# Performance work log

Hardware: AMD Instinct MI355X
Metric: run time of the kernel (lower is better)

The kernel has to match this reference:

```python
import jax, jax.numpy as jnp
import numpy as np


def setup_inputs() -> dict:
    key = jax.random.key(0)
    ks = jax.random.split(key, 7)
    B, D, d1, d2, d3 = 256, 256, 1024, 512, 256
    s = lambda f: 1.0 / np.sqrt(f)  # torch nn.Linear-style init scale
    return {
        "x": jax.random.normal(ks[0], (B, D), jnp.float32),
        "W1": jax.random.normal(ks[1], (d1, D), jnp.float32) * s(D),
        "b1": jax.random.normal(ks[2], (d1,), jnp.float32) * s(D),
        "W2": jax.random.normal(ks[3], (d2, d1), jnp.float32) * s(d1),
        "b2": jax.random.normal(ks[4], (d2,), jnp.float32) * s(d1),
        "W3": jax.random.normal(ks[5], (d3, d2), jnp.float32) * s(d2),
        "b3": jax.random.normal(ks[6], (d3,), jnp.float32) * s(d2),
        "k": 10,
    }


def _border_dists(x, W1, b1, W2, b2, W3, b3):
    # Layer 1: pre-activations and boundary distances. For the first layer the
    # effective linear map is W1 itself (shared across the batch).
    z1 = x @ W1.T + b1                                   # [B, d1]
    dist1 = jnp.abs(z1) / jnp.linalg.norm(W1, axis=1)    # [B, d1]
    m1 = (z1 > 0).astype(x.dtype)
    V1 = m1[:, :, None] * W1[None]                       # [B, d1, D] per-instance map after ReLU
    h1 = m1 * z1

    # Layer 2
    z2 = h1 @ W2.T + b2                                  # [B, d2]
    V2 = jnp.einsum('oi,bid->bod', W2, V1)               # [B, d2, D]
    dist2 = jnp.abs(z2) / jnp.linalg.norm(V2, axis=2)
    m2 = (z2 > 0).astype(x.dtype)
    h2 = m2 * z2

    # Layer 3
    z3 = h2 @ W3.T + b3                                  # [B, d3]
    V3 = jnp.einsum('oi,bid->bod', W3, m2[:, :, None] * V2)  # [B, d3, D]
    dist3 = jnp.abs(z3) / jnp.linalg.norm(V3, axis=2)

    return jnp.concatenate([dist1, dist2, dist3], axis=1)  # [B, d1+d2+d3]


def reference(x, W1, b1, W2, b2, W3, b3, k):
    dists = _border_dists(x, W1, b1, W2, b2, W3, b3)
    # smallest-k distances per instance via top_k on negated distances
    neg_top, _ = jax.lax.top_k(-dists, k)                # [B, k]
    return jnp.sum(-neg_top)                             # border-distance loss (scalar)
```

## Files before the change

kernel.cpp:

```cpp
#include <hip/hip_runtime.h>
#include <math.h>
#include <float.h>

#define B   256
#define D   256
#define D1  1024
#define D2  512
#define D3  256
#define NDIST (D1 + D2 + D3)
#define CQ  2.0f

typedef __attribute__((ext_vector_type(8))) short short8;
typedef __attribute__((ext_vector_type(4))) float f32x4;
typedef __attribute__((ext_vector_type(4))) int   i32x4;

__device__ __forceinline__ float waveReduceSum(float v) {
    #pragma unroll
    for (int off = 32; off > 0; off >>= 1)
        v += __shfl_down(v, off, 64);
    return v;
}
__device__ __forceinline__ float waveReduceMax(float v) {
    #pragma unroll
    for (int off = 32; off > 0; off >>= 1)
        v = fmaxf(v, __shfl_down(v, off, 64));
    return v;
}
__device__ __forceinline__ unsigned short f2bf(float f) {
    unsigned int u = __float_as_uint(f);
    u = (u + 0x7FFFu + ((u >> 16) & 1u)) >> 16;
    return (unsigned short)u;
}
__device__ __forceinline__ float bf2f(unsigned short h) {
    return __uint_as_float(((unsigned int)h) << 16);
}
__device__ __forceinline__ void gld16(const void* g, void* l) {
    __builtin_amdgcn_global_load_lds(
        (const __attribute__((address_space(1))) unsigned int*)g,
        (__attribute__((address_space(3))) unsigned int*)l, 16, 0, 0);
}
__device__ __forceinline__ int swz_src(int row, int lane) {
    return ((lane & 3) + ((row >> 1) & 3)) & 3;
}
__device__ __forceinline__ int swz_frag(int row, int quad) {
    return row * 32 + (((quad - ((row >> 1) & 3)) & 3) * 8);
}

__device__ __forceinline__ void split_job(const float* src, unsigned short* hi,
                                          unsigned short* lo, int off) {
    float4 v = *(const float4*)(src + off);
    ushort4 h, l;
    h.x = f2bf(v.x); l.x = f2bf(v.x - bf2f(h.x));
    h.y = f2bf(v.y); l.y = f2bf(v.y - bf2f(h.y));
    h.z = f2bf(v.z); l.z = f2bf(v.z - bf2f(h.z));
    h.w = f2bf(v.w); l.w = f2bf(v.w - bf2f(h.w));
    *(ushort4*)(hi + off) = h;
    *(ushort4*)(lo + off) = l;
}

__global__ __launch_bounds__(256) void k_prepA(
    const float* __restrict__ x, const float* __restrict__ W1,
    unsigned short* __restrict__ xhi,  unsigned short* __restrict__ xlo,
    unsigned short* __restrict__ W1hi, unsigned short* __restrict__ W1lo,
    float* __restrict__ rn1) {
    int blk = blockIdx.x;
    int t = threadIdx.x;
    if (blk < 64) {
        split_job(x, xhi, xlo, blk * 1024 + t * 4);
        return;
    }
    if (blk < 320) {
        split_job(W1, W1hi, W1lo, (blk - 64) * 1024 + t * 4);
        return;
    }
    {
        int gw = (blk - 320) * 4 + (t >> 6);
        int lane = t & 63;
        const float* row = W1 + (size_t)gw * D;
        float s = 0.f;
        for (int tt = lane; tt < D; tt += 64) { float v = row[tt]; s += v * v; }
        s = waveReduceSum(s);
        if (lane == 0) rn1[gw] = sqrtf(s);
    }
}

template <int KD, int KL>
__device__ __forceinline__ void mfma3_64(
    const unsigned short* __restrict__ Ahi, const unsigned short* __restrict__ Alo,
    const unsigned short* __restrict__ Bhi, const unsigned short* __restrict__ Blo,
    int m0, int n0, int k0, unsigned short* sm, f32x4 acc[2][2]) {
    int tid = threadIdx.x;
    int l = tid & 63, w = tid >> 6;
    int rsub = l >> 2;
    int quad = l >> 4, l16 = l & 15;
    int wm = (w >> 1) * 32, wn = (w & 1) * 32;
    unsigned short* sAh = sm;
    unsigned short* sAl = sm + 2048;
    unsigned short* sBh = sm + 4096;
    unsigned short* sBl = sm + 6144;
    ptrdiff_t dA = Alo - Ahi, dB = Blo - Bhi;
    int rloc = w * 16 + rsub;
    int c = swz_src(rloc, l);
    const unsigned short* pa = Ahi + (size_t)(m0 + rloc) * KD + k0 + c * 8;
    const unsigned short* pb = Bhi + (size_t)(n0 + rloc) * KD + k0 + c * 8;
    int aoff[2], boff[2];
    #pragma unroll
    for (int mt = 0; mt < 2; mt++) aoff[mt] = swz_frag(wm + mt * 16 + l16, quad);
    #pragma unroll
    for (int nt = 0; nt < 2; nt++) boff[nt] = swz_frag(wn + nt * 16 + l16, quad);
    for (int kk = 0; kk < KL; kk += 32) {
        gld16(pa + kk,      sAh + w * 512);
        gld16(pa + dA + kk, sAl + w * 512);
        gld16(pb + kk,      sBh + w * 512);
        gld16(pb + dB + kk, sBl + w * 512);
        __syncthreads();
        short8 ah[2], al[2], bh[2], bl[2];
        #pragma unroll
        for (int mt = 0; mt < 2; mt++) {
            ah[mt] = *(const short8*)(sAh + aoff[mt]);
            al[mt] = *(const short8*)(sAl + aoff[mt]);
        }
        #pragma unroll
        for (int nt = 0; nt < 2; nt++) {
            bh[nt] = *(const short8*)(sBh + boff[nt]);
            bl[nt] = *(const short8*)(sBl + boff[nt]);
        }
        #pragma unroll
        for (int mt = 0; mt < 2; mt++)
            #pragma unroll
            for (int nt = 0; nt < 2; nt++) {
                acc[mt][nt] = __builtin_amdgcn_mfma_f32_16x16x32_bf16(ah[mt], bh[nt], acc[mt][nt], 0, 0, 0);
                acc[mt][nt] = __builtin_amdgcn_mfma_f32_16x16x32_bf16(ah[mt], bl[nt], acc[mt][nt], 0, 0, 0);
                acc[mt][nt] = __builtin_amdgcn_mfma_f32_16x16x32_bf16(al[mt], bh[nt], acc[mt][nt], 0, 0, 0);
            }
        __syncthreads();
    }
}

__global__ __launch_bounds__(256) void k_l1p(
    const float* __restrict__ W1, const float* __restrict__ W2,
    const float* __restrict__ W3,
    const unsigned short* __restrict__ xhi,  const unsigned short* __restrict__ xlo,
    const unsigned short* __restrict__ W1hi, const unsigned short* __restrict__ W1lo,
    const float* __restrict__ b1, const float* __restrict__ rn1,
    float* __restrict__ dists, unsigned char* __restrict__ m1q,
    unsigned short* __restrict__ h1hi, unsigned short* __restrict__ h1lo,
    float* __restrict__ zeros, float* __restrict__ outp,
    unsigned short* __restrict__ W2hi, unsigned short* __restrict__ W2lo,
    unsigned short* __restrict__ W3hi, unsigned short* __restrict__ W3lo,
    signed char* __restrict__ W1Ti8, float* __restrict__ saq,
    signed char* __restrict__ W2i8,  float* __restrict__ sbq,
    signed char* __restrict__ W3i8,  float* __restrict__ s3q) {
    __shared__ __align__(16) unsigned short sm[8192];
    int blk = blockIdx.x;
    int t = threadIdx.x;

    if (blk < 64) {
        int m0 = (blk & 3) * 64, n0 = (blk >> 2) * 64;
        f32x4 acc[2][2] = {};
        mfma3_64<D, D>(xhi, xlo, W1hi, W1lo, m0, n0, 0, sm, acc);
        int l = t & 63, w = t >> 6;
        int quad = l >> 4, l16 = l & 15;
        int wm = (w >> 1) * 32, wn = (w & 1) * 32;
        #pragma unroll
        for (int mt = 0; mt < 2; mt++)
            #pragma unroll
            for (int nt = 0; nt < 2; nt++) {
                int n = n0 + wn + nt * 16 + l16;
                float bv = b1[n], rv = rn1[n];
                #pragma unroll
                for (int r = 0; r < 4; r++) {
                    int m = m0 + wm + mt * 16 + quad * 4 + r;
                    float z = acc[mt][nt][r] + bv;
                    size_t idx = (size_t)m * D1 + n;
                    dists[idx] = fabsf(z) / rv;
                    m1q[idx] = (z > 0.f) ? 0xFFu : 0u;
                    float h = z > 0.f ? z : 0.f;
                    unsigned short hh = f2bf(h);
                    h1hi[idx] = hh;
                    h1lo[idx] = f2bf(h - bf2f(hh));
                }
            }
        return;
    }
    if (blk < 448) {
        if (blk == 64 && t == 0) outp[0] = 0.f;
        int i4 = (blk - 64) * 1024 + t * 4;
        *(float4*)(zeros + i4) = make_float4(0.f, 0.f, 0.f, 0.f);
        return;
    }
    if (blk < 960) {
        split_job(W2, W2hi, W2lo, (blk - 448) * 1024 + t * 4);
        return;
    }
    if (blk < 1088) {
        split_job(W3, W3hi, W3lo, (blk - 960) * 1024 + t * 4);
        return;
    }
    if (blk < 1120) {
        int ty = t >> 5, tx = t & 31;
        int d = (blk - 1088) * 8 + ty;
        float m = 0.f;
        for (int i = tx; i < D1; i += 32) m = fmaxf(m, fabsf(W1[(size_t)i * D + d]));
        #pragma unroll
        for (int off = 16; off > 0; off >>= 1) m = fmaxf(m, __shfl_down(m, off, 32));
        m = __shfl(m, 0, 32);
        m = fmaxf(m, 1e-20f);
        if (tx == 0) saq[d] = m / 127.f;
        float inv = 127.f / m;
        for (int i = tx; i < D1; i += 32) {
            int q = __float2int_rn(W1[(size_t)i * D + d] * inv);
            W1Ti8[(size_t)d * D1 + i] = (signed char)q;
        }
        return;
    }
    if (blk < 1248) {
        int o = (blk - 1120) * 4 + (t >> 6);
        int l = t & 63;
        const float* row = W2 + (size_t)o * D1;
        float m = 0.f;
        for (int tt = l; tt < D1; tt += 64) m = fmaxf(m, fabsf(row[tt]));
        m = waveReduceMax(m);
        m = __shfl(m, 0, 64);
        m = fmaxf(m, 1e-20f);
        if (l == 0) sbq[o] = m / 127.f;
        float inv = 127.f / m;
        for (int tt = l; tt < D1; tt += 64)
            W2i8[(size_t)o * D1 + tt] = (signed char)__float2int_rn(row[tt] * inv);
        return;
    }
    {
        int p = (blk - 1248) * 4 + (t >> 6);
        int l = t & 63;
        const float* row = W3 + (size_t)p * D2;
        float m = 0.f;
        for (int tt = l; tt < D2; tt += 64) m = fmaxf(m, fabsf(row[tt]));
        m = waveReduceMax(m);
        m = __shfl(m, 0, 64);
        m = fmaxf(m, 1e-20f);
        if (l == 0) s3q[p] = m / 127.f;
        float inv = 127.f / m;
        for (int tt = l; tt < D2; tt += 64)
            W3i8[(size_t)p * D2 + tt] = (signed char)__float2int_rn(row[tt] * inv);
    }
}

__global__ __launch_bounds__(256) void k_big1(
    const unsigned short* __restrict__ h1hi, const unsigned short* __restrict__ h1lo,
    const unsigned short* __restrict__ W2hi, const unsigned short* __restrict__ W2lo,
    float* __restrict__ z2,
    const signed char* __restrict__ W1Ti8,
    const signed char* __restrict__ W2i8,
    const unsigned char* __restrict__ m1q,
    const float* __restrict__ saq,
    const float* __restrict__ sbq,
    signed char* __restrict__ qV2,
    float* __restrict__ norm2) {
    __shared__ __align__(16) unsigned char smem[32768];
    int bid = blockIdx.x;

    if (bid < 128) {
        unsigned short* sm = (unsigned short*)smem;
        int m0 = (bid & 3) * 64, n0 = ((bid >> 2) & 7) * 64, k0 = (bid >> 5) * 256;
        f32x4 acc[2][2] = {};
        mfma3_64<D1, 256>(h1hi, h1lo, W2hi, W2lo, m0, n0, k0, sm, acc);
        int l = threadIdx.x & 63, w = threadIdx.x >> 6;
        int quad = l >> 4, l16 = l & 15;
        int wm = (w >> 1) * 32, wn = (w & 1) * 32;
        #pragma unroll
        for (int mt = 0; mt < 2; mt++)
            #pragma unroll
            for (int nt = 0; nt < 2; nt++) {
                int n = n0 + wn + nt * 16 + l16;
                #pragma unroll
                for (int r = 0; r < 4; r++) {
                    int m = m0 + wm + mt * 16 + quad * 4 + r;
                    atomicAdd(&z2[(size_t)m * D2 + n], acc[mt][nt][r]);
                }
            }
        return;
    }

    int j = bid - 128;
    signed char* As = (signed char*)smem;
    signed char* Bs = (signed char*)smem + 16384;
    int m0 = (j & 1) * 128;
    int o0 = ((j >> 1) & 3) * 128;
    int b = j >> 3;
    int tid = threadIdx.x;
    int l = tid & 63, w = tid >> 6;
    int quad = l >> 4, l16 = l & 15;
    int wm = (w >> 1) * 64, wn = (w & 1) * 64;
    const unsigned char* mrow = m1q + (size_t)b * D1;

    const signed char* pa[4];
    const signed char* pb[4];
    int lrow = l >> 3, ls = l & 7;
    #pragma unroll
    for (int r = 0; r < 4; r++) {
        int row = r * 32 + w * 8 + lrow;
        int c = (ls + (row & 7)) & 7;
        pa[r] = W1Ti8 + (size_t)(m0 + row) * D1 + c * 16;
        pb[r] = W2i8 + (size_t)(o0 + row) * D1 + c * 16;
    }
    int aoff[4][2], boff[4][2];
    #pragma unroll
    for (int mt = 0; mt < 4; mt++) {
        int tr = wm + mt * 16 + l16;
        #pragma unroll
        for (int ks = 0; ks < 2; ks++)
            aoff[mt][ks] = tr * 128 + (((ks * 4 + quad) - (tr & 7)) & 7) * 16;
    }
    #pragma unroll
    for (int nt = 0; nt < 4; nt++) {
        int tr = wn + nt * 16 + l16;
        #pragma unroll
        for (int ks = 0; ks < 2; ks++)
            boff[nt][ks] = tr * 128 + (((ks * 4 + quad) - (tr & 7)) & 7) * 16;
    }

    i32x4 acc[4][4];
    #pragma unroll
    for (int i = 0; i < 4; i++)
        #pragma unroll
        for (int jj = 0; jj < 4; jj++) acc[i][jj] = (i32x4)0;

    for (int kk = 0; kk < D1; kk += 128) {
        #pragma unroll
        for (int r = 0; r < 4; r++) {
            gld16(pa[r] + kk, As + r * 4096 + w * 1024);
            gld16(pb[r] + kk, Bs + r * 4096 + w * 1024);
        }
        i32x4 mv0 = *(const i32x4*)(mrow + kk + quad * 16);
        i32x4 mv1 = *(const i32x4*)(mrow + kk + 64 + quad * 16);
        __syncthreads();
        #pragma unroll
        for (int ks = 0; ks < 2; ks++) {
            i32x4 mv = ks ? mv1 : mv0;
            i32x4 a[4], bq[4];
            #pragma unroll
            for (int mt = 0; mt < 4; mt++)
                a[mt] = (*(const i32x4*)(As + aoff[mt][ks])) & mv;
            #pragma unroll
            for (int nt = 0; nt < 4; nt++)
                bq[nt] = *(const i32x4*)(Bs + boff[nt][ks]);
            #pragma unroll
            for (int mt = 0; mt < 4; mt++)
                #pragma unroll
                for (int nt = 0; nt < 4; nt++)
                    acc[mt][nt] = __builtin_amdgcn_mfma_i32_16x16x64_i8(
                        a[mt], bq[nt], acc[mt][nt], 0, 0, 0);
        }
        __syncthreads();
    }

    float sad[4][4];
    #pragma unroll
    for (int mt = 0; mt < 4; mt++)
        #pragma unroll
        for (int r = 0; r < 4; r++)
            sad[mt][r] = saq[m0 + wm + mt * 16 + quad * 4 + r];
    float sbv[4], sbdq[4];
    #pragma unroll
    for (int nt = 0; nt < 4; nt++) {
        sbv[nt] = sbq[o0 + wn + nt * 16 + l16];
        sbdq[nt] = sbv[nt] * (1.0f / CQ);
    }

    #pragma unroll
    for (int nt = 0; nt < 4; nt++) {
        float s = 0.f;
        #pragma unroll
        for (int mt = 0; mt < 4; mt++)
            #pragma unroll
            for (int r = 0; r < 4; r++) {
                float v = (float)acc[mt][nt][r] * sad[mt][r] * sbv[nt];
                s += v * v;
            }
        s += __shfl_down(s, 32, 64);
        s += __shfl_down(s, 16, 64);
        if (l < 16)
            atomicAdd(&norm2[(size_t)b * D2 + o0 + wn + nt * 16 + l], s);
    }

    signed char* qb = qV2 + (size_t)b * (D * D2);
    #pragma unroll
    for (int mt = 0; mt < 4; mt++) {
        int dbase = m0 + wm + mt * 16 + quad * 4;
        #pragma unroll
        for (int r = 0; r < 4; r++)
            #pragma unroll
            for (int nt = 0; nt < 4; nt++) {
                int o = o0 + wn + nt * 16 + l16;
                int qi = __float2int_rn((float)acc[mt][nt][r] * sbdq[nt]);
                qi = max(-127, min(127, qi));
                qb[(size_t)(dbase + r) * D2 + o] = (signed char)qi;
            }
    }
}

__global__ __launch_bounds__(256) void k_big2(
    const float* __restrict__ z2,
    const float* __restrict__ b2,
    const unsigned short* __restrict__ W3hi, const unsigned short* __restrict__ W3lo,
    float* __restrict__ z3,
    const signed char* __restrict__ W3i8,
    const signed char* __restrict__ qV2,
    const float* __restrict__ saq,
    const float* __restrict__ s3q,
    float* __restrict__ norm3) {
    __shared__ __align__(16) unsigned char smem[33280];
    int bid = blockIdx.x;
    int tid = threadIdx.x;

    if (bid < 32) {
        unsigned short* sAh = (unsigned short*)smem;
        unsigned short* sAl = sAh + 2048;
        unsigned short* sBh = sAh + 4096;
        unsigned short* sBl = sAh + 6144;
        int m0 = (bid & 3) * 64, n0 = ((bid >> 2) & 3) * 64, k0 = (bid >> 4) * 256;
        int l = tid & 63, w = tid >> 6;
        int rsub = l >> 2;
        int quad = l >> 4, l16 = l & 15;
        int wm = (w >> 1) * 32, wn = (w & 1) * 32;
        int rloc = w * 16 + rsub;
        int c = swz_src(rloc, l);
        const float* pz  = z2 + (size_t)(m0 + rloc) * D2 + k0 + c * 8;
        const float* pbi = b2 + k0 + c * 8;
        const unsigned short* pb = W3hi + (size_t)(n0 + rloc) * D2 + k0 + c * 8;
        ptrdiff_t dB = W3lo - W3hi;
        int aoff[2], boff[2];
        #pragma unroll
        for (int mt = 0; mt < 2; mt++) aoff[mt] = swz_frag(wm + mt * 16 + l16, quad);
        #pragma unroll
        for (int nt = 0; nt < 2; nt++) boff[nt] = swz_frag(wn + nt * 16 + l16, quad);
        int wrA = w * 512 + l * 8;
        f32x4 acc[2][2] = {};
        for (int kk = 0; kk < 256; kk += 32) {
            gld16(pb + kk,      sBh + w * 512);
            gld16(pb + dB + kk, sBl + w * 512);
            float4 za = *(const float4*)(pz + kk);
            float4 zb = *(const float4*)(pz + kk + 4);
            float4 ba = *(const float4*)(pbi + kk);
            float4 bb = *(const float4*)(pbi + kk + 4);
            float hv[8] = { za.x + ba.x, za.y + ba.y, za.z + ba.z, za.w + ba.w,
                            zb.x + bb.x, zb.y + bb.y, zb.z + bb.z, zb.w + bb.w };
            short8 h8, l8;
            #pragma unroll
            for (int q2 = 0; q2 < 8; q2++) {
                float h = hv[q2] > 0.f ? hv[q2] : 0.f;
                unsigned short hh = f2bf(h);
                h8[q2] = (short)hh;
                l8[q2] = (short)f2bf(h - bf2f(hh));
            }
            *(short8*)(sAh + wrA) = h8;
            *(short8*)(sAl + wrA) = l8;
            __syncthreads();
            short8 ah[2], al[2], bh[2], bl[2];
            #pragma unroll
            for (int mt = 0; mt < 2; mt++) {
                ah[mt] = *(const short8*)(sAh + aoff[mt]);
                al[mt] = *(const short8*)(sAl + aoff[mt]);
            }
            #pragma unroll
            for (int nt = 0; nt < 2; nt++) {
                bh[nt] = *(const short8*)(sBh + boff[nt]);
                bl[nt] = *(const short8*)(sBl + boff[nt]);
            }
            #pragma unroll
            for (int mt = 0; mt < 2; mt++)
                #pragma unroll
                for (int nt = 0; nt < 2; nt++) {
                    acc[mt][nt] = __builtin_amdgcn_mfma_f32_16x16x32_bf16(ah[mt], bh[nt], acc[mt][nt], 0, 0, 0);
                    acc[mt][nt] = __builtin_amdgcn_mfma_f32_16x16x32_bf16(ah[mt], bl[nt], acc[mt][nt], 0, 0, 0);
                    acc[mt][nt] = __builtin_amdgcn_mfma_f32_16x16x32_bf16(al[mt], bh[nt], acc[mt][nt], 0, 0, 0);
                }
            __syncthreads();
        }
        #pragma unroll
        for (int mt = 0; mt < 2; mt++)
            #pragma unroll
            for (int nt = 0; nt < 2; nt++) {
                int n = n0 + wn + nt * 16 + l16;
                #pragma unroll
                for (int r = 0; r < 4; r++) {
                    int m = m0 + wm + mt * 16 + quad * 4 + r;
                    atomicAdd(&z3[(size_t)m * D3 + n], acc[mt][nt][r]);
                }
            }
        return;
    }

    int j = bid - 32;
    signed char* As = (signed char*)smem;
    signed char* Bs = (signed char*)smem + 16384;
    unsigned char* mbuf = (unsigned char*)smem + 32768;
    int m0 = (j & 1) * 128;
    int n0 = ((j >> 1) & 1) * 128;
    int bc = j >> 2;
    int l = tid & 63, w = tid >> 6;
    int quad = l >> 4, l16 = l & 15;
    int wm = (w >> 1) * 64, wn = (w & 1) * 64;
    const signed char* Bsrc = qV2 + (size_t)bc * (D * D2);

    {
        #pragma unroll
        for (int rr = 0; rr < 2; rr++) {
            int o = tid * 2 + rr;
            float z = z2[(size_t)bc * D2 + o] + b2[o];
            mbuf[o] = (z > 0.f) ? 0xFFu : 0u;
        }
    }
    __syncthreads();

    const signed char* pa[4];
    const signed char* pb[4];
    int lrow = l >> 3, ls = l & 7;
    #pragma unroll
    for (int r = 0; r < 4; r++) {
        int row = r * 32 + w * 8 + lrow;
        int c = (ls + (row & 7)) & 7;
        pa[r] = W3i8 + (size_t)(m0 + row) * D2 + c * 16;
        pb[r] = Bsrc + (size_t)(n0 + row) * D2 + c * 16;
    }
    int aoff[4][2], boff[4][2];
    #pragma unroll
    for (int mt = 0; mt < 4; mt++) {
        int tr = wm + mt * 16 + l16;
        #pragma unroll
        for (int ks = 0; ks < 2; ks++)
            aoff[mt][ks] = tr * 128 + (((ks * 4 + quad) - (tr & 7)) & 7) * 16;
    }
    #pragma unroll
    for (int nt = 0; nt < 4; nt++) {
        int tr = wn + nt * 16 + l16;
        #pragma unroll
        for (int ks = 0; ks < 2; ks++)
            boff[nt][ks] = tr * 128 + (((ks * 4 + quad) - (tr & 7)) & 7) * 16;
    }

    i32x4 acc[4][4];
    #pragma unroll
    for (int i = 0; i < 4; i++)
        #pragma unroll
        for (int jj = 0; jj < 4; jj++) acc[i][jj] = (i32x4)0;

    for (int kk = 0; kk < D2; kk += 128) {
        #pragma unroll
        for (int r = 0; r < 4; r++) {
            gld16(pa[r] + kk, As + r * 4096 + w * 1024);
            gld16(pb[r] + kk, Bs + r * 4096 + w * 1024);
        }
        __syncthreads();
        i32x4 mv0 = *(const i32x4*)(mbuf + kk + quad * 16);
        i32x4 mv1 = *(const i32x4*)(mbuf + kk + 64 + quad * 16);
        #pragma unroll
        for (int ks = 0; ks < 2; ks++) {
            i32x4 mv = ks ? mv1 : mv0;
            i32x4 a[4], bq[4];
            #pragma unroll
            for (int mt = 0; mt < 4; mt++)
                a[mt] = *(const i32x4*)(As + aoff[mt][ks]);
            #pragma unroll
            for (int nt = 0; nt < 4; nt++)
                bq[nt] = (*(const i32x4*)(Bs + boff[nt][ks])) & mv;
            #pragma unroll
            for (int mt = 0; mt < 4; mt++)
                #pragma unroll
                for (int nt = 0; nt < 4; nt++)
                    acc[mt][nt] = __builtin_amdgcn_mfma_i32_16x16x64_i8(
                        a[mt], bq[nt], acc[mt][nt], 0, 0, 0);
        }
        __syncthreads();
    }

    float saCQ[4];
    #pragma unroll
    for (int nt = 0; nt < 4; nt++)
        saCQ[nt] = saq[n0 + wn + nt * 16 + l16] * CQ;

    #pragma unroll
    for (int mt = 0; mt < 4; mt++)
        #pragma unroll
        for (int r = 0; r < 4; r++) {
            float s = 0.f;
            #pragma unroll
            for (int nt = 0; nt < 4; nt++) {
                float v = (float)acc[mt][nt][r] * saCQ[nt];
                s += v * v;
            }
            s += __shfl_down(s, 8, 64);
            s += __shfl_down(s, 4, 64);
            s += __shfl_down(s, 2, 64);
            s += __shfl_down(s, 1, 64);
            if (l16 == 0) {
                int p = m0 + wm + mt * 16 + quad * 4 + r;
                float s3 = s3q[p];
                atomicAdd(&norm3[(size_t)bc * D3 + p], s * s3 * s3);
            }
        }
}

__global__ __launch_bounds__(256) void k_topk(
    const float* __restrict__ dists,
    const float* __restrict__ z2, const float* __restrict__ b2,
    const float* __restrict__ norm2,
    const float* __restrict__ z3, const float* __restrict__ b3,
    const float* __restrict__ norm3,
    const int* __restrict__ kp, float* __restrict__ outp) {
    int t = threadIdx.x;
    int wv = t >> 6, lane = t & 63;
    int b = blockIdx.x * 4 + wv;
    float lv[28];
    #pragma unroll
    for (int j = 0; j < 16; j++)
        lv[j] = dists[(size_t)b * D1 + lane + 64 * j];
    #pragma unroll
    for (int j = 16; j < 24; j++) {
        int o = lane + 64 * (j - 16);
        float zz = z2[(size_t)b * D2 + o] + b2[o];
        lv[j] = fabsf(zz) / sqrtf(norm2[(size_t)b * D2 + o]);
    }
    #pragma unroll
    for (int j = 24; j < 28; j++) {
        int p = lane + 64 * (j - 24);
        float zz = z3[(size_t)b * D3 + p] + b3[p];
        lv[j] = fabsf(zz) / sqrtf(norm3[(size_t)b * D3 + p]);
    }
    int k = *kp;
    if (k > NDIST) k = NDIST;
    float sum = 0.f;
    for (int it = 0; it < k; it++) {
        float mv = lv[0]; int mj = 0;
        #pragma unroll
        for (int j = 1; j < 28; j++)
            if (lv[j] < mv) { mv = lv[j]; mj = j; }
        unsigned long long key =
            ((unsigned long long)__float_as_uint(mv) << 32) | (unsigned)(lane * 32 + mj);
        #pragma unroll
        for (int off = 1; off < 64; off <<= 1) {
            unsigned long long o = __shfl_xor(key, off, 64);
            if (o < key) key = o;
        }
        sum += __uint_as_float((unsigned)(key >> 32));
        int wl = (int)((key >> 5) & 63u), wj = (int)(key & 31u);
        if (lane == wl) lv[wj] = FLT_MAX;
    }
    if (lane == 0) atomicAdd(outp, sum);
}

extern "C" void kernel_launch(void* const* d_in, const int* in_sizes, int n_in,
                              void* d_out, int out_size, void* d_ws, size_t ws_size,
                              hipStream_t stream) {
    const float* x  = (const float*)d_in[0];
    const float* W1 = (const float*)d_in[1];
    const float* b1 = (const float*)d_in[2];
    const float* W2 = (const float*)d_in[3];
    const float* b2 = (const float*)d_in[4];
    const float* W3 = (const float*)d_in[5];
    const float* b3 = (const float*)d_in[6];
    const int*   kp = (const int*)d_in[7];
    float* outp = (float*)d_out;

    float* fp = (float*)d_ws;
    float* rn1     = fp;                          fp += D1;
    float* dists   = fp;                          fp += (size_t)B * D1;
    float* saq     = fp;                          fp += D;
    float* sbq     = fp;                          fp += D2;
    float* s3q     = fp;                          fp += D3;
    float* z2      = fp;                          fp += (size_t)B * D2;
    float* z3      = fp;                          fp += (size_t)B * D3;
    float* norm2   = fp;                          fp += (size_t)B * D2;
    float* norm3   = fp;                          fp += (size_t)B * D3;
    unsigned short* up = (unsigned short*)fp;
    unsigned short* W2hi  = up;  up += (size_t)D2 * D1;
    unsigned short* W2lo  = up;  up += (size_t)D2 * D1;
    unsigned short* W3hi  = up;  up += (size_t)D3 * D2;
    unsigned short* W3lo  = up;  up += (size_t)D3 * D2;
    unsigned short* xhi   = up;  up += (size_t)B * D;
    unsigned short* xlo   = up;  up += (size_t)B * D;
    unsigned short* W1hi  = up;  up += (size_t)D1 * D;
    unsigned short* W1lo  = up;  up += (size_t)D1 * D;
    unsigned short* h1hi  = up;  up += (size_t)B * D1;
    unsigned short* h1lo  = up;  up += (size_t)B * D1;
    signed char*    cp = (signed char*)up;
    signed char*    W1Ti8 = cp;  cp += (size_t)D * D1;
    signed char*    W2i8  = cp;  cp += (size_t)D2 * D1;
    signed char*    W3i8  = cp;  cp += (size_t)D3 * D2;
    unsigned char*  m1q   = (unsigned char*)cp;  cp += (size_t)B * D1;
    signed char*    qV2   = cp;

    k_prepA<<<576, 256, 0, stream>>>(x, W1, xhi, xlo, W1hi, W1lo, rn1);

    k_l1p<<<1312, 256, 0, stream>>>(W1, W2, W3, xhi, xlo, W1hi, W1lo, b1, rn1,
                                    dists, m1q, h1hi, h1lo,
                                    z2, outp, W2hi, W2lo, W3hi, W3lo,
                                    W1Ti8, saq, W2i8, sbq, W3i8, s3q);

    k_big1<<<2176, 256, 0, stream>>>(h1hi, h1lo, W2hi, W2lo, z2,
                                     W1Ti8, W2i8, m1q, saq, sbq, qV2, norm2);

    k_big2<<<1056, 256, 0, stream>>>(z2, b2, W3hi, W3lo, z3,
                                     W3i8, qV2, saq, s3q, norm3);

    k_topk<<<B / 4, 256, 0, stream>>>(dists, z2, b2, norm2, z3, b3, norm3, kp, outp);
}
```

Baseline: 177.9 us.

## Fuse bf16 split of x and W1 into layer-1 GEMM, drop prep kernel

Removes the separate k_prepA launch. The layer-1 GEMM blocks now load fp32 x and W1 directly and split them into bf16 hi/lo inside the K loop before staging to shared memory. The W1 row-norm computation moves to extra blocks of k_l1p, and the division by rn1 is deferred to k_topk, which removes the dependency between the two. This saves one kernel launch and the round trip of the hi/lo intermediates through global memory, at the cost of redundant conversion work in each GEMM block and no double-buffering in the inlined loop.

```diff
diff --git a/kernel.cpp b/kernel.cpp
--- a/kernel.cpp
+++ b/kernel.cpp
@@ -58,29 +58,15 @@
     *(ushort4*)(lo + off) = l;
 }
 
-__global__ __launch_bounds__(256) void k_prepA(
-    const float* __restrict__ x, const float* __restrict__ W1,
-    unsigned short* __restrict__ xhi,  unsigned short* __restrict__ xlo,
-    unsigned short* __restrict__ W1hi, unsigned short* __restrict__ W1lo,
-    float* __restrict__ rn1) {
-    int blk = blockIdx.x;
-    int t = threadIdx.x;
-    if (blk < 64) {
-        split_job(x, xhi, xlo, blk * 1024 + t * 4);
-        return;
-    }
-    if (blk < 320) {
-        split_job(W1, W1hi, W1lo, (blk - 64) * 1024 + t * 4);
-        return;
-    }
-    {
-        int gw = (blk - 320) * 4 + (t >> 6);
-        int lane = t & 63;
-        const float* row = W1 + (size_t)gw * D;
-        float s = 0.f;
-        for (int tt = lane; tt < D; tt += 64) { float v = row[tt]; s += v * v; }
-        s = waveReduceSum(s);
-        if (lane == 0) rn1[gw] = sqrtf(s);
+__device__ __forceinline__ void split8(const float* p, short8& h8, short8& l8) {
+    float4 a = *(const float4*)(p);
+    float4 b = *(const float4*)(p + 4);
+    float hv[8] = { a.x, a.y, a.z, a.w, b.x, b.y, b.z, b.w };
+    #pragma unroll
+    for (int q = 0; q < 8; q++) {
+        unsigned short hh = f2bf(hv[q]);
+        h8[q] = (short)hh;
+        l8[q] = (short)f2bf(hv[q] - bf2f(hh));
     }
 }
 
@@ -138,11 +124,9 @@
 }
 
 __global__ __launch_bounds__(256) void k_l1p(
-    const float* __restrict__ W1, const float* __restrict__ W2,
-    const float* __restrict__ W3,
-    const unsigned short* __restrict__ xhi,  const unsigned short* __restrict__ xlo,
-    const unsigned short* __restrict__ W1hi, const unsigned short* __restrict__ W1lo,
-    const float* __restrict__ b1, const float* __restrict__ rn1,
+    const float* __restrict__ x, const float* __restrict__ W1,
+    const float* __restrict__ W2, const float* __restrict__ W3,
+    const float* __restrict__ b1,
     float* __restrict__ dists, unsigned char* __restrict__ m1q,
     unsigned short* __restrict__ h1hi, unsigned short* __restrict__ h1lo,
     float* __restrict__ zeros, float* __restrict__ outp,
@@ -150,30 +134,75 @@
     unsigned short* __restrict__ W3hi, unsigned short* __restrict__ W3lo,
     signed char* __restrict__ W1Ti8, float* __restrict__ saq,
     signed char* __restrict__ W2i8,  float* __restrict__ sbq,
-    signed char* __restrict__ W3i8,  float* __restrict__ s3q) {
+    signed char* __restrict__ W3i8,  float* __restrict__ s3q,
+    float* __restrict__ rn1) {
     __shared__ __align__(16) unsigned short sm[8192];
     int blk = blockIdx.x;
     int t = threadIdx.x;
 
     if (blk < 64) {
+        unsigned short* sAh = sm;
+        unsigned short* sAl = sm + 2048;
+        unsigned short* sBh = sm + 4096;
+        unsigned short* sBl = sm + 6144;
         int m0 = (blk & 3) * 64, n0 = (blk >> 2) * 64;
-        f32x4 acc[2][2] = {};
-        mfma3_64<D, D>(xhi, xlo, W1hi, W1lo, m0, n0, 0, sm, acc);
         int l = t & 63, w = t >> 6;
+        int rsub = l >> 2;
         int quad = l >> 4, l16 = l & 15;
         int wm = (w >> 1) * 32, wn = (w & 1) * 32;
+        int rloc = w * 16 + rsub;
+        int c = swz_src(rloc, l);
+        const float* pax = x + (size_t)(m0 + rloc) * D + c * 8;
+        const float* pbw = W1 + (size_t)(n0 + rloc) * D + c * 8;
+        int aoff[2], boff[2];
+        #pragma unroll
+        for (int mt = 0; mt < 2; mt++) aoff[mt] = swz_frag(wm + mt * 16 + l16, quad);
+        #pragma unroll
+        for (int nt = 0; nt < 2; nt++) boff[nt] = swz_frag(wn + nt * 16 + l16, quad);
+        int wrA = w * 512 + l * 8;
+        f32x4 acc[2][2] = {};
+        for (int kk = 0; kk < D; kk += 32) {
+            short8 ha, la, hb, lb;
+            split8(pax + kk, ha, la);
+            split8(pbw + kk, hb, lb);
+            *(short8*)(sAh + wrA) = ha;
+            *(short8*)(sAl + wrA) = la;
+            *(short8*)(sBh + wrA) = hb;
+            *(short8*)(sBl + wrA) = lb;
+            __syncthreads();
+            short8 ah[2], al[2], bh[2], bl[2];
+            #pragma unroll
+            for (int mt = 0; mt < 2; mt++) {
+                ah[mt] = *(const short8*)(sAh + aoff[mt]);
+                al[mt] = *(const short8*)(sAl + aoff[mt]);
+            }
+            #pragma unroll
+            for (int nt = 0; nt < 2; nt++) {
+                bh[nt] = *(const short8*)(sBh + boff[nt]);
+                bl[nt] = *(const short8*)(sBl + boff[nt]);
+            }
+            #pragma unroll
+            for (int mt = 0; mt < 2; mt++)
+                #pragma unroll
+                for (int nt = 0; nt < 2; nt++) {
+                    acc[mt][nt] = __builtin_amdgcn_mfma_f32_16x16x32_bf16(ah[mt], bh[nt], acc[mt][nt], 0, 0, 0);
+                    acc[mt][nt] = __builtin_amdgcn_mfma_f32_16x16x32_bf16(ah[mt], bl[nt], acc[mt][nt], 0, 0, 0);
+                    acc[mt][nt] = __builtin_amdgcn_mfma_f32_16x16x32_bf16(al[mt], bh[nt], acc[mt][nt], 0, 0, 0);
+                }
+            __syncthreads();
+        }
         #pragma unroll
         for (int mt = 0; mt < 2; mt++)
             #pragma unroll
             for (int nt = 0; nt < 2; nt++) {
                 int n = n0 + wn + nt * 16 + l16;
-                float bv = b1[n], rv = rn1[n];
+                float bv = b1[n];
                 #pragma unroll
                 for (int r = 0; r < 4; r++) {
                     int m = m0 + wm + mt * 16 + quad * 4 + r;
                     float z = acc[mt][nt][r] + bv;
                     size_t idx = (size_t)m * D1 + n;
-                    dists[idx] = fabsf(z) / rv;
+                    dists[idx] = fabsf(z);
                     m1q[idx] = (z > 0.f) ? 0xFFu : 0u;
                     float h = z > 0.f ? z : 0.f;
                     unsigned short hh = f2bf(h);
@@ -229,7 +258,7 @@
             W2i8[(size_t)o * D1 + tt] = (signed char)__float2int_rn(row[tt] * inv);
         return;
     }
-    {
+    if (blk < 1312) {
         int p = (blk - 1248) * 4 + (t >> 6);
         int l = t & 63;
         const float* row = W3 + (size_t)p * D2;
@@ -242,6 +271,16 @@
         float inv = 127.f / m;
         for (int tt = l; tt < D2; tt += 64)
             W3i8[(size_t)p * D2 + tt] = (signed char)__float2int_rn(row[tt] * inv);
+        return;
+    }
+    {
+        int gw = (blk - 1312) * 4 + (t >> 6);
+        int lane = t & 63;
+        const float* row = W1 + (size_t)gw * D;
+        float s = 0.f;
+        for (int tt = lane; tt < D; tt += 64) { float v = row[tt]; s += v * v; }
+        s = waveReduceSum(s);
+        if (lane == 0) rn1[gw] = sqrtf(s);
     }
 }
 
@@ -603,6 +642,7 @@
 
 __global__ __launch_bounds__(256) void k_topk(
     const float* __restrict__ dists,
+    const float* __restrict__ rn1,
     const float* __restrict__ z2, const float* __restrict__ b2,
     const float* __restrict__ norm2,
     const float* __restrict__ z3, const float* __restrict__ b3,
@@ -613,8 +653,10 @@
     int b = blockIdx.x * 4 + wv;
     float lv[28];
     #pragma unroll
-    for (int j = 0; j < 16; j++)
-        lv[j] = dists[(size_t)b * D1 + lane + 64 * j];
+    for (int j = 0; j < 16; j++) {
+        int n = lane + 64 * j;
+        lv[j] = dists[(size_t)b * D1 + n] / rn1[n];
+    }
     #pragma unroll
     for (int j = 16; j < 24; j++) {
         int o = lane + 64 * (j - 16);
@@ -677,10 +719,6 @@
     unsigned short* W2lo  = up;  up += (size_t)D2 * D1;
     unsigned short* W3hi  = up;  up += (size_t)D3 * D2;
     unsigned short* W3lo  = up;  up += (size_t)D3 * D2;
-    unsigned short* xhi   = up;  up += (size_t)B * D;
-    unsigned short* xlo   = up;  up += (size_t)B * D;
-    unsigned short* W1hi  = up;  up += (size_t)D1 * D;
-    unsigned short* W1lo  = up;  up += (size_t)D1 * D;
     unsigned short* h1hi  = up;  up += (size_t)B * D1;
     unsigned short* h1lo  = up;  up += (size_t)B * D1;
     signed char*    cp = (signed char*)up;
@@ -690,12 +728,10 @@
     unsigned char*  m1q   = (unsigned char*)cp;  cp += (size_t)B * D1;
     signed char*    qV2   = cp;
 
-    k_prepA<<<576, 256, 0, stream>>>(x, W1, xhi, xlo, W1hi, W1lo, rn1);
-
-    k_l1p<<<1312, 256, 0, stream>>>(W1, W2, W3, xhi, xlo, W1hi, W1lo, b1, rn1,
+    k_l1p<<<1568, 256, 0, stream>>>(x, W1, W2, W3, b1,
                                     dists, m1q, h1hi, h1lo,
                                     z2, outp, W2hi, W2lo, W3hi, W3lo,
-                                    W1Ti8, saq, W2i8, sbq, W3i8, s3q);
+                                    W1Ti8, saq, W2i8, sbq, W3i8, s3q, rn1);
 
     k_big1<<<2176, 256, 0, stream>>>(h1hi, h1lo, W2hi, W2lo, z2,
                                      W1Ti8, W2i8, m1q, saq, sbq, qV2, norm2);
@@ -703,5 +739,6 @@
     k_big2<<<1056, 256, 0, stream>>>(z2, b2, W3hi, W3lo, z3,
                                      W3i8, qV2, saq, s3q, norm3);
 
-    k_topk<<<B / 4, 256, 0, stream>>>(dists, z2, b2, norm2, z3, b3, norm3, kp, outp);
-}
+    k_topk<<<B / 4, 256, 0, stream>>>(dists, rn1, z2, b2, norm2, z3, b3, norm3,
+                                      kp, outp);
+}
```

After: 175.4 us. No clear change (-1.4%).
